# Performance work log

Measured on AMD Instinct MI355X. Metric: run time of the kernel, lower is better.

The kernel has to match this reference:

```python
import jax, jax.numpy as jnp
import numpy as np

L = 8        # num_layers
REPEAT = 2   # repeats per layer
DIM = 256    # mixer hidden dim
DIM2 = 128   # head dim (divisible by 32 for AvgPool1d(32))
B = 8192
EPS = 1e-5


def hardswish(x):
    return x * jnp.clip(x + 3.0, 0.0, 6.0) * (1.0 / 6.0)


def layernorm(x, g, b):
    m = jnp.mean(x, axis=-1, keepdims=True)
    xc = x - m
    v = jnp.mean(xc * xc, axis=-1, keepdims=True)
    return xc * jax.lax.rsqrt(v + EPS) * g + b


def setup_inputs() -> dict:
    key = jax.random.key(0)
    ks = jax.random.split(key, 32)
    s = 0.1
    inp = {
        "x": jax.random.normal(ks[0], (B, 3, 32, 32), dtype=jnp.float32),
        "conv_w": jax.random.normal(ks[1], (3,), dtype=jnp.float32) * s,
        "conv_b": jax.random.normal(ks[2], (1,), dtype=jnp.float32) * s,
        "fc0_w": jax.random.normal(ks[3], (32, 32), dtype=jnp.float32) * s,
        "fc0_b": jax.random.normal(ks[4], (32,), dtype=jnp.float32) * s,
        "ln1_g": jnp.ones((L, 32), dtype=jnp.float32),
        "ln1_b": jnp.zeros((L, 32), dtype=jnp.float32),
        "w11": jax.random.normal(ks[5], (L, DIM, 32), dtype=jnp.float32) * s,
        "b11": jax.random.normal(ks[6], (L, DIM), dtype=jnp.float32) * s,
        "w12": jax.random.normal(ks[7], (L, 32, DIM), dtype=jnp.float32) * s,
        "b12": jax.random.normal(ks[8], (L, 32), dtype=jnp.float32) * s,
        "ln2_g": jnp.ones((L, 32), dtype=jnp.float32),
        "ln2_b": jnp.zeros((L, 32), dtype=jnp.float32),
        "w21": jax.random.normal(ks[9], (L, DIM, 32), dtype=jnp.float32) * s,
        "b21": jax.random.normal(ks[10], (L, DIM), dtype=jnp.float32) * s,
        "w22": jax.random.normal(ks[11], (L, 32, DIM), dtype=jnp.float32) * s,
        "b22": jax.random.normal(ks[12], (L, 32), dtype=jnp.float32) * s,
        "fc1_w": jax.random.normal(ks[13], (DIM2, 32), dtype=jnp.float32) * s,
        "fc1_b": jax.random.normal(ks[14], (DIM2,), dtype=jnp.float32) * s,
        "fcout_w": jax.random.normal(ks[15], (10, DIM2), dtype=jnp.float32) * s,
        "fcout_b": jax.random.normal(ks[16], (10,), dtype=jnp.float32) * s,
    }
    return inp


def reference(x, conv_w, conv_b, fc0_w, fc0_b, ln1_g, ln1_b, w11, b11, w12, b12,
              ln2_g, ln2_b, w21, b21, w22, b22, fc1_w, fc1_b, fcout_w, fcout_b):
    # rgb_conv: 1x1 conv 3->1 channels, then squeeze -> [B, 32, 32]
    h = jnp.einsum('bchw,c->bhw', x, conv_w) + conv_b[0]
    h = h @ fc0_w.T + fc0_b  # fc0 over last dim (32)

    for i in range(L):
        for _ in range(REPEAT):
            # token-mixing branch (operates along dim 1 via permute)
            t = layernorm(h, ln1_g[i], ln1_b[i])
            t = jnp.swapaxes(t, 1, 2)                      # [B, 32, 32]
            t = hardswish(t @ w11[i].T + b11[i])           # [B, 32, DIM]
            t = t @ w12[i].T + b12[i]                      # [B, 32, 32]
            h = h + jnp.swapaxes(t, 1, 2)
            # channel-mixing branch
            c = layernorm(h, ln2_g[i], ln2_b[i])
            c = hardswish(c @ w21[i].T + b21[i])           # [B, 32, DIM]
            h = h + (c @ w22[i].T + b22[i])                # [B, 32, 32]

    y = hardswish(h @ fc1_w.T + fc1_b)                     # [B, 32, DIM2]
    # AvgPool1d(kernel=32, stride=32) over last dim -> [B, 32, DIM2//32]
    y = y.reshape(y.shape[0], 32, DIM2 // 32, 32).mean(axis=-1)
    y = y.reshape(y.shape[0], -1)                          # [B, DIM2]
    return y @ fcout_w.T + fcout_b                         # [B, 10]
```

## Files before the change

kernel.cpp:

```cpp
#include <hip/hip_runtime.h>

#define LNUM 8

typedef __attribute__((ext_vector_type(4))) float f32x4;
typedef __attribute__((ext_vector_type(2))) float f32x2;
typedef __attribute__((ext_vector_type(8))) _Float16 f16x8;
typedef __attribute__((ext_vector_type(2))) _Float16 f16x2;

#define MFMAH(A,B,C) __builtin_amdgcn_mfma_f32_16x16x32_f16(A,B,C,0,0,0)

#define PKRTZ(a,b) __builtin_bit_cast(f16x2, __builtin_amdgcn_cvt_pkrtz(a,b))

__device__ __forceinline__ float hswish_clamp(float t) {
  return __builtin_amdgcn_fmed3f(t + 3.f, 0.f, 6.f);
}

__device__ __forceinline__ int hws(int row, int c) {
  return (row << 5) + ((((c >> 2) ^ (row & 7)) << 2) | (c & 3));
}

__global__ void prep_weights(const float* __restrict__ w11, const float* __restrict__ b11,
                             const float* __restrict__ w12, const float* __restrict__ b12,
                             const float* __restrict__ g1,  const float* __restrict__ be1,
                             const float* __restrict__ w21, const float* __restrict__ b21,
                             const float* __restrict__ w22, const float* __restrict__ b22,
                             const float* __restrict__ g2,  const float* __restrict__ be2,
                             char* __restrict__ ws)
{
  const int lb = blockIdx.x;
  const int lay = lb >> 1, br = lb & 1;
  const float* w1  = (br ? w21 : w11) + lay*8192;
  const float* w2  = (br ? w22 : w12) + lay*8192;
  const float* bb1 = (br ? b21 : b11) + lay*256;
  const float* bb2 = (br ? b22 : b12) + lay*32;
  const float* gg  = (br ? g2  : g1 ) + lay*32;
  const float* bb  = (br ? be2 : be1) + lay*32;
  char* o = ws + (size_t)lb * 34816;
  _Float16* w1f = (_Float16*)o;
  _Float16* w2f = (_Float16*)(o + 16384);
  float* pr  = (float*)(o + 32768);
  const int t = threadIdx.x;
  #pragma unroll
  for (int i = 0; i < 4; ++i) {
    int s = t + i*256;
    int lane = s & 63;
    int row = (s >> 6)*16 + (lane & 15);
    int kb  = ((lane >> 4) & 3) * 8;
    const float* src = w1 + row*32 + kb;
    #pragma unroll
    for (int j = 0; j < 8; ++j) w1f[s*8 + j] = (_Float16)src[j];
  }
  #pragma unroll
  for (int i = 0; i < 4; ++i) {
    int s = t + i*256;
    int lane = s & 63;
    int tt = s >> 7;
    int nt = (s >> 6) & 1;
    int n  = nt*16 + (lane & 15);
    int qq = (lane >> 4) & 3;
    const float* src = w2 + n*256 + tt*32 + qq*4;
    _Float16* dst = w2f + s*8;
    #pragma unroll
    for (int j = 0; j < 4; ++j) dst[j]     = (_Float16)(src[j]      * (1.0f/6.0f));
    #pragma unroll
    for (int j = 0; j < 4; ++j) dst[4 + j] = (_Float16)(src[16 + j] * (1.0f/6.0f));
  }
  pr[t] = bb1[t];
  if (t < 32)      pr[256 + t] = bb2[t];
  else if (t < 64) pr[256 + t] = gg[t - 32];
  else if (t < 96) pr[256 + t] = bb[t - 64];
}

__global__ __launch_bounds__(256, 4)
void mixer_mfma(const float* __restrict__ x,
                const float* __restrict__ conv_w, const float* __restrict__ conv_b,
                const float* __restrict__ fc0_w,  const float* __restrict__ fc0_b,
                const char*  __restrict__ ws,
                const float* __restrict__ fc1_w,  const float* __restrict__ fc1_b,
                const float* __restrict__ fcout_w, const float* __restrict__ fcout_b,
                float* __restrict__ out)
{
  __shared__ float smem[4 * 2176];
  const int tid = threadIdx.x;
  const int wv  = tid >> 6;
  const int lid = tid & 63;
  const int ml  = lid & 15;
  const int q   = lid >> 4;
  const int q4  = q << 2, q8 = q << 3;
  const int sl  = lid >> 5, r = lid & 31;
  const int r7  = r & 7;

  float* hW  = smem + wv * 2176;
  float* stW = hW + 2048;

  const size_t b0 = (size_t)blockIdx.x * 8 + (size_t)wv * 2;

  {
    const size_t b = b0 + sl;
    const float* xb = x + b*3072 + r*32;
    const float cw0 = conv_w[0], cw1 = conv_w[1], cw2 = conv_w[2], cb = conv_b[0];
    float g[32];
    #pragma unroll
    for (int j4 = 0; j4 < 8; ++j4) {
      f32x4 a0 = *(const f32x4*)(xb + j4*4);
      f32x4 a1 = *(const f32x4*)(xb + 1024 + j4*4);
      f32x4 a2 = *(const f32x4*)(xb + 2048 + j4*4);
      #pragma unroll
      for (int e = 0; e < 4; ++e)
        g[j4*4+e] = cw0*a0[e] + cw1*a1[e] + cw2*a2[e] + cb;
    }
    f32x4* hp = (f32x4*)(hW + sl*1024 + (r << 5));
    #pragma unroll
    for (int a = 0; a < 8; ++a) {
      f32x4 w;
      #pragma unroll
      for (int e = 0; e < 4; ++e) {
        const int j = a*4 + e;
        const float* wr = fc0_w + j*32;
        float acc = fc0_b[j];
        #pragma unroll
        for (int k = 0; k < 32; ++k) acc += g[k]*wr[k];
        w[e] = acc;
      }
      hp[a ^ r7] = w;
    }
  }

  for (int lay = 0; lay < LNUM; ++lay)
  for (int rep = 0; rep < 2; ++rep)
  for (int br = 0; br < 2; ++br) {
    const char* wsb = ws + (size_t)(lay*2 + br) * 34816;
    const f16x8* w1f = (const f16x8*)wsb;
    const f16x8* w2f = (const f16x8*)(wsb + 16384);
    const float* pb1 = (const float*)(wsb + 32768);
    const float* pb2 = pb1 + 256;
    const float* pg  = pb1 + 288;
    const float* pbt = pb1 + 320;

    {
      const f32x4* hp = (const f32x4*)(hW + sl*1024 + (r << 5));
      float sum = 0.f, sq = 0.f;
      #pragma unroll
      for (int a = 0; a < 8; ++a) {
        f32x4 v = hp[a ^ r7];
        #pragma unroll
        for (int e = 0; e < 4; ++e) { sum += v[e]; sq += v[e]*v[e]; }
      }
      float m = sum * (1.f/32.f);
      float rstd = rsqrtf(sq*(1.f/32.f) - m*m + 1e-5f);
      *(f32x2*)(stW + ((sl << 5) + r)*2) = (f32x2){m, rstd};
    }

    f16x8 b1[4];
    if (br == 0) {
      const float ga = pg[ml],  gb = pg[16 + ml];
      const float ba = pbt[ml], bb2v = pbt[16 + ml];
      #pragma unroll
      for (int i = 0; i < 8; ++i) {
        const int k = q8 + i;
        f32x2 s0 = *(const f32x2*)(stW + k*2);
        f32x2 s1 = *(const f32x2*)(stW + 64 + k*2);
        #pragma unroll
        for (int mt = 0; mt < 4; ++mt) {
          const int samp = mt >> 1;
          const int c = ((mt & 1) << 4) + ml;
          f32x2 st = samp ? s1 : s0;
          float v = hW[samp*1024 + hws(k, c)];
          float g_ = (mt & 1) ? gb : ga;
          float be = (mt & 1) ? bb2v : ba;
          b1[mt][i] = (_Float16)((v - st[0]) * st[1] * g_ + be);
        }
      }
    } else {
      f32x4 g0 = *(const f32x4*)(pg + q8);
      f32x4 g1 = *(const f32x4*)(pg + q8 + 4);
      f32x4 t0 = *(const f32x4*)(pbt + q8);
      f32x4 t1 = *(const f32x4*)(pbt + q8 + 4);
      #pragma unroll
      for (int mt = 0; mt < 4; ++mt) {
        const int samp = mt >> 1;
        const int row = ((mt & 1) << 4) + ml;
        f32x2 st = *(const f32x2*)(stW + ((samp << 5) + row)*2);
        const f32x4* hr = (const f32x4*)(hW + samp*1024 + (row << 5));
        f32x4 v0 = hr[(2*q)     ^ (row & 7)];
        f32x4 v1 = hr[(2*q + 1) ^ (row & 7)];
        #pragma unroll
        for (int e = 0; e < 4; ++e) {
          b1[mt][e]     = (_Float16)((v0[e] - st[0]) * st[1] * g0[e] + t0[e]);
          b1[mt][4 + e] = (_Float16)((v1[e] - st[0]) * st[1] * g1[e] + t1[e]);
        }
      }
    }

    f32x4 acc2[2][4];
    {
      f32x4 i0 = *(const f32x4*)(pb2 + q4);
      f32x4 i1 = *(const f32x4*)(pb2 + 16 + q4);
      #pragma unroll
      for (int mt = 0; mt < 4; ++mt) { acc2[0][mt] = i0; acc2[1][mt] = i1; }
    }
    #pragma unroll 2
    for (int t = 0; t < 8; ++t) {
      f16x8 a1a = w1f[(t*2 + 0)*64 + lid];
      f16x8 a1b = w1f[(t*2 + 1)*64 + lid];
      f32x4 biasa = *(const f32x4*)(pb1 + t*32 + q4);
      f32x4 biasb = *(const f32x4*)(pb1 + t*32 + 16 + q4);
      f16x8 a2a = w2f[(t*2 + 0)*64 + lid];
      f16x8 a2b = w2f[(t*2 + 1)*64 + lid];
      #pragma unroll
      for (int mt = 0; mt < 4; ++mt) {
        f32x4 c1a = MFMAH(a1a, b1[mt], biasa);
        f32x4 c1b = MFMAH(a1b, b1[mt], biasb);
        float va0 = c1a[0]*hswish_clamp(c1a[0]);
        float va1 = c1a[1]*hswish_clamp(c1a[1]);
        float va2 = c1a[2]*hswish_clamp(c1a[2]);
        float va3 = c1a[3]*hswish_clamp(c1a[3]);
        float vb0 = c1b[0]*hswish_clamp(c1b[0]);
        float vb1 = c1b[1]*hswish_clamp(c1b[1]);
        float vb2 = c1b[2]*hswish_clamp(c1b[2]);
        float vb3 = c1b[3]*hswish_clamp(c1b[3]);
        union { f16x2 h2[4]; f16x8 v; } b2u;
        b2u.h2[0] = PKRTZ(va0, va1);
        b2u.h2[1] = PKRTZ(va2, va3);
        b2u.h2[2] = PKRTZ(vb0, vb1);
        b2u.h2[3] = PKRTZ(vb2, vb3);
        acc2[0][mt] = MFMAH(a2a, b2u.v, acc2[0][mt]);
        acc2[1][mt] = MFMAH(a2b, b2u.v, acc2[1][mt]);
      }
    }

    if (br == 0) {
      #pragma unroll
      for (int mt = 0; mt < 4; ++mt) {
        const int samp = mt >> 1;
        const int c = ((mt & 1) << 4) + ml;
        float* hs = hW + samp*1024;
        #pragma unroll
        for (int nt = 0; nt < 2; ++nt)
        #pragma unroll
        for (int rg = 0; rg < 4; ++rg) {
          const int n = (nt << 4) + q4 + rg;
          hs[hws(n, c)] += acc2[nt][mt][rg];
        }
      }
    } else {
      #pragma unroll
      for (int mt = 0; mt < 4; ++mt) {
        const int samp = mt >> 1;
        const int row = ((mt & 1) << 4) + ml;
        f32x4* hr = (f32x4*)(hW + samp*1024 + (row << 5));
        #pragma unroll
        for (int nt = 0; nt < 2; ++nt) {
          const int a = ((nt << 2) + q) ^ (row & 7);
          f32x4 v = hr[a];
          v += acc2[nt][mt];
          hr[a] = v;
        }
      }
    }
  }

  {
    const size_t b = b0 + sl;
    float hv[32];
    {
      const f32x4* hp = (const f32x4*)(hW + sl*1024 + (r << 5));
      #pragma unroll
      for (int a = 0; a < 8; ++a) {
        f32x4 v = hp[a ^ r7];
        #pragma unroll
        for (int e = 0; e < 4; ++e) hv[a*4 + e] = v[e];
      }
    }
    float pooled[4];
    #pragma unroll
    for (int c = 0; c < 4; ++c) {
      float accp = 0.f;
      for (int e2 = 0; e2 < 32; ++e2) {
        const float* wr = fc1_w + (c*32 + e2)*32;
        float acc = fc1_b[c*32 + e2];
        #pragma unroll
        for (int k = 0; k < 32; ++k) acc += hv[k]*wr[k];
        accp += acc * hswish_clamp(acc) * (1.f/6.f);
      }
      pooled[c] = accp * (1.f/32.f);
    }
    float* pf = hW + sl*1024;
    #pragma unroll
    for (int c = 0; c < 4; ++c) pf[r*4 + c] = pooled[c];
    if (r < 10) {
      const float* pv = hW + sl*1024;
      const float* wr = fcout_w + r*128;
      float acc = fcout_b[r];
      #pragma unroll 8
      for (int m = 0; m < 128; ++m) acc += pv[m]*wr[m];
      out[b*10 + r] = acc;
    }
  }
}

extern "C" void kernel_launch(void* const* d_in, const int* in_sizes, int n_in,
                              void* d_out, int out_size, void* d_ws, size_t ws_size,
                              hipStream_t stream) {
  (void)in_sizes; (void)n_in; (void)out_size; (void)ws_size;
  const float* x       = (const float*)d_in[0];
  const float* conv_w  = (const float*)d_in[1];
  const float* conv_b  = (const float*)d_in[2];
  const float* fc0_w   = (const float*)d_in[3];
  const float* fc0_b   = (const float*)d_in[4];
  const float* ln1_g   = (const float*)d_in[5];
  const float* ln1_b   = (const float*)d_in[6];
  const float* w11     = (const float*)d_in[7];
  const float* b11     = (const float*)d_in[8];
  const float* w12     = (const float*)d_in[9];
  const float* b12     = (const float*)d_in[10];
  const float* ln2_g   = (const float*)d_in[11];
  const float* ln2_b   = (const float*)d_in[12];
  const float* w21     = (const float*)d_in[13];
  const float* b21     = (const float*)d_in[14];
  const float* w22     = (const float*)d_in[15];
  const float* b22     = (const float*)d_in[16];
  const float* fc1_w   = (const float*)d_in[17];
  const float* fc1_b   = (const float*)d_in[18];
  const float* fcout_w = (const float*)d_in[19];
  const float* fcout_b = (const float*)d_in[20];
  float* out = (float*)d_out;
  char* ws = (char*)d_ws;

  prep_weights<<<16, 256, 0, stream>>>(w11, b11, w12, b12, ln1_g, ln1_b,
                                       w21, b21, w22, b22, ln2_g, ln2_b, ws);
  mixer_mfma<<<1024, 256, 0, stream>>>(x, conv_w, conv_b, fc0_w, fc0_b,
                                       (const char*)ws, fc1_w, fc1_b,
                                       fcout_w, fcout_b, out);
}
```

Before: 487.2 us.

## Process one sample per wave, use MFMA for fc1 head and packed fp16 hardswish

Each wave now handles one sample instead of two, which halves shared memory per block and doubles the grid, with launch bounds raised to 8 blocks per CU. The fc0 stage is spread across both half-waves. The fc1/pool head moves from a scalar fp32 loop to fp16 MFMA, using a weight layout prepared by an extra prep block. The hardswish between the two MFMA layers is now done in packed fp16 after conversion. This trades some precision and per-wave MFMA density for more occupancy and a cheaper epilogue.

```diff
diff --git a/kernel.cpp b/kernel.cpp
--- a/kernel.cpp
+++ b/kernel.cpp
@@ -8,11 +8,18 @@
 typedef __attribute__((ext_vector_type(2))) _Float16 f16x2;
 
 #define MFMAH(A,B,C) __builtin_amdgcn_mfma_f32_16x16x32_f16(A,B,C,0,0,0)
-
 #define PKRTZ(a,b) __builtin_bit_cast(f16x2, __builtin_amdgcn_cvt_pkrtz(a,b))
 
 __device__ __forceinline__ float hswish_clamp(float t) {
   return __builtin_amdgcn_fmed3f(t + 3.f, 0.f, 6.f);
+}
+__device__ __forceinline__ f16x2 hsw_pk(f16x2 t) {
+  const f16x2 c3 = {(_Float16)3.0f, (_Float16)3.0f};
+  const f16x2 c0 = {(_Float16)0.0f, (_Float16)0.0f};
+  const f16x2 c6 = {(_Float16)6.0f, (_Float16)6.0f};
+  f16x2 u = t + c3;
+  u = __builtin_elementwise_min(__builtin_elementwise_max(u, c0), c6);
+  return t * u;
 }
 
 __device__ __forceinline__ int hws(int row, int c) {
@@ -25,9 +32,28 @@
                              const float* __restrict__ w21, const float* __restrict__ b21,
                              const float* __restrict__ w22, const float* __restrict__ b22,
                              const float* __restrict__ g2,  const float* __restrict__ be2,
+                             const float* __restrict__ fc1w, const float* __restrict__ fc1b,
                              char* __restrict__ ws)
 {
   const int lb = blockIdx.x;
+  const int t = threadIdx.x;
+  if (lb == 16) {
+    char* o = ws + (size_t)16 * 34816;
+    _Float16* wf = (_Float16*)o;
+    float* pr = (float*)(o + 8192);
+    #pragma unroll
+    for (int i = 0; i < 2; ++i) {
+      int s = t + i*256;
+      int lane = s & 63;
+      int row = (s >> 6)*16 + (lane & 15);
+      int kb  = ((lane >> 4) & 3) * 8;
+      const float* src = fc1w + row*32 + kb;
+      #pragma unroll
+      for (int j = 0; j < 8; ++j) wf[s*8 + j] = (_Float16)src[j];
+    }
+    if (t < 128) pr[t] = fc1b[t];
+    return;
+  }
   const int lay = lb >> 1, br = lb & 1;
   const float* w1  = (br ? w21 : w11) + lay*8192;
   const float* w2  = (br ? w22 : w12) + lay*8192;
@@ -39,7 +65,6 @@
   _Float16* w1f = (_Float16*)o;
   _Float16* w2f = (_Float16*)(o + 16384);
   float* pr  = (float*)(o + 32768);
-  const int t = threadIdx.x;
   #pragma unroll
   for (int i = 0; i < 4; ++i) {
     int s = t + i*256;
@@ -71,16 +96,15 @@
   else if (t < 96) pr[256 + t] = bb[t - 64];
 }
 
-__global__ __launch_bounds__(256, 4)
+__global__ __launch_bounds__(256, 8)
 void mixer_mfma(const float* __restrict__ x,
                 const float* __restrict__ conv_w, const float* __restrict__ conv_b,
                 const float* __restrict__ fc0_w,  const float* __restrict__ fc0_b,
                 const char*  __restrict__ ws,
-                const float* __restrict__ fc1_w,  const float* __restrict__ fc1_b,
                 const float* __restrict__ fcout_w, const float* __restrict__ fcout_b,
                 float* __restrict__ out)
 {
-  __shared__ float smem[4 * 2176];
+  __shared__ float smem[4 * 1088];
   const int tid = threadIdx.x;
   const int wv  = tid >> 6;
   const int lid = tid & 63;
@@ -90,39 +114,44 @@
   const int sl  = lid >> 5, r = lid & 31;
   const int r7  = r & 7;
 
-  float* hW  = smem + wv * 2176;
-  float* stW = hW + 2048;
-
-  const size_t b0 = (size_t)blockIdx.x * 8 + (size_t)wv * 2;
+  float* hW  = smem + wv * 1088;
+  float* stW = hW + 1024;
+
+  const size_t b = (size_t)blockIdx.x * 4 + (size_t)wv;
 
   {
-    const size_t b = b0 + sl;
     const float* xb = x + b*3072 + r*32;
     const float cw0 = conv_w[0], cw1 = conv_w[1], cw2 = conv_w[2], cb = conv_b[0];
-    float g[32];
-    #pragma unroll
-    for (int j4 = 0; j4 < 8; ++j4) {
-      f32x4 a0 = *(const f32x4*)(xb + j4*4);
-      f32x4 a1 = *(const f32x4*)(xb + 1024 + j4*4);
-      f32x4 a2 = *(const f32x4*)(xb + 2048 + j4*4);
-      #pragma unroll
-      for (int e = 0; e < 4; ++e)
-        g[j4*4+e] = cw0*a0[e] + cw1*a1[e] + cw2*a2[e] + cb;
-    }
-    f32x4* hp = (f32x4*)(hW + sl*1024 + (r << 5));
+    f32x4* hp = (f32x4*)(hW + (r << 5));
+    #pragma unroll
+    for (int cc = 0; cc < 4; ++cc) {
+      const int a = sl*4 + cc;
+      f32x4 a0 = *(const f32x4*)(xb + a*4);
+      f32x4 a1 = *(const f32x4*)(xb + 1024 + a*4);
+      f32x4 a2 = *(const f32x4*)(xb + 2048 + a*4);
+      f32x4 g4;
+      #pragma unroll
+      for (int e = 0; e < 4; ++e) g4[e] = cw0*a0[e] + cw1*a1[e] + cw2*a2[e] + cb;
+      hp[a ^ r7] = g4;
+    }
+    float accs[16];
+    #pragma unroll
+    for (int jj = 0; jj < 16; ++jj) accs[jj] = fc0_b[sl*16 + jj];
     #pragma unroll
     for (int a = 0; a < 8; ++a) {
-      f32x4 w;
-      #pragma unroll
-      for (int e = 0; e < 4; ++e) {
-        const int j = a*4 + e;
-        const float* wr = fc0_w + j*32;
-        float acc = fc0_b[j];
-        #pragma unroll
-        for (int k = 0; k < 32; ++k) acc += g[k]*wr[k];
-        w[e] = acc;
-      }
-      hp[a ^ r7] = w;
+      f32x4 g4 = hp[a ^ r7];
+      #pragma unroll
+      for (int jj = 0; jj < 16; ++jj) {
+        const f32x4 w4 = *(const f32x4*)(fc0_w + (sl*16 + jj)*32 + a*4);
+        accs[jj] += g4[0]*w4[0] + g4[1]*w4[1] + g4[2]*w4[2] + g4[3]*w4[3];
+      }
+    }
+    #pragma unroll
+    for (int cc = 0; cc < 4; ++cc) {
+      f32x4 w4;
+      #pragma unroll
+      for (int e = 0; e < 4; ++e) w4[e] = accs[cc*4 + e];
+      hp[(sl*4 + cc) ^ r7] = w4;
     }
   }
 
@@ -138,7 +167,7 @@
     const float* pbt = pb1 + 320;
 
     {
-      const f32x4* hp = (const f32x4*)(hW + sl*1024 + (r << 5));
+      const f32x4* hp = (const f32x4*)(hW + (r << 5));
       float sum = 0.f, sq = 0.f;
       #pragma unroll
       for (int a = 0; a < 8; ++a) {
@@ -148,28 +177,21 @@
       }
       float m = sum * (1.f/32.f);
       float rstd = rsqrtf(sq*(1.f/32.f) - m*m + 1e-5f);
-      *(f32x2*)(stW + ((sl << 5) + r)*2) = (f32x2){m, rstd};
-    }
-
-    f16x8 b1[4];
+      *(f32x2*)(stW + r*2) = (f32x2){m, rstd};
+    }
+
+    f16x8 b1[2];
     if (br == 0) {
       const float ga = pg[ml],  gb = pg[16 + ml];
       const float ba = pbt[ml], bb2v = pbt[16 + ml];
       #pragma unroll
       for (int i = 0; i < 8; ++i) {
         const int k = q8 + i;
-        f32x2 s0 = *(const f32x2*)(stW + k*2);
-        f32x2 s1 = *(const f32x2*)(stW + 64 + k*2);
-        #pragma unroll
-        for (int mt = 0; mt < 4; ++mt) {
-          const int samp = mt >> 1;
-          const int c = ((mt & 1) << 4) + ml;
-          f32x2 st = samp ? s1 : s0;
-          float v = hW[samp*1024 + hws(k, c)];
-          float g_ = (mt & 1) ? gb : ga;
-          float be = (mt & 1) ? bb2v : ba;
-          b1[mt][i] = (_Float16)((v - st[0]) * st[1] * g_ + be);
-        }
+        f32x2 st = *(const f32x2*)(stW + k*2);
+        float v0 = hW[hws(k, ml)];
+        float v1 = hW[hws(k, 16 + ml)];
+        b1[0][i] = (_Float16)((v0 - st[0]) * st[1] * ga + ba);
+        b1[1][i] = (_Float16)((v1 - st[0]) * st[1] * gb + bb2v);
       }
     } else {
       f32x4 g0 = *(const f32x4*)(pg + q8);
@@ -177,11 +199,10 @@
       f32x4 t0 = *(const f32x4*)(pbt + q8);
       f32x4 t1 = *(const f32x4*)(pbt + q8 + 4);
       #pragma unroll
-      for (int mt = 0; mt < 4; ++mt) {
-        const int samp = mt >> 1;
-        const int row = ((mt & 1) << 4) + ml;
-        f32x2 st = *(const f32x2*)(stW + ((samp << 5) + row)*2);
-        const f32x4* hr = (const f32x4*)(hW + samp*1024 + (row << 5));
+      for (int mt = 0; mt < 2; ++mt) {
+        const int row = (mt << 4) + ml;
+        f32x2 st = *(const f32x2*)(stW + row*2);
+        const f32x4* hr = (const f32x4*)(hW + (row << 5));
         f32x4 v0 = hr[(2*q)     ^ (row & 7)];
         f32x4 v1 = hr[(2*q + 1) ^ (row & 7)];
         #pragma unroll
@@ -192,12 +213,12 @@
       }
     }
 
-    f32x4 acc2[2][4];
+    f32x4 acc2[2][2];
     {
       f32x4 i0 = *(const f32x4*)(pb2 + q4);
       f32x4 i1 = *(const f32x4*)(pb2 + 16 + q4);
       #pragma unroll
-      for (int mt = 0; mt < 4; ++mt) { acc2[0][mt] = i0; acc2[1][mt] = i1; }
+      for (int mt = 0; mt < 2; ++mt) { acc2[0][mt] = i0; acc2[1][mt] = i1; }
     }
     #pragma unroll 2
     for (int t = 0; t < 8; ++t) {
@@ -208,22 +229,14 @@
       f16x8 a2a = w2f[(t*2 + 0)*64 + lid];
       f16x8 a2b = w2f[(t*2 + 1)*64 + lid];
       #pragma unroll
-      for (int mt = 0; mt < 4; ++mt) {
+      for (int mt = 0; mt < 2; ++mt) {
         f32x4 c1a = MFMAH(a1a, b1[mt], biasa);
         f32x4 c1b = MFMAH(a1b, b1[mt], biasb);
-        float va0 = c1a[0]*hswish_clamp(c1a[0]);
-        float va1 = c1a[1]*hswish_clamp(c1a[1]);
-        float va2 = c1a[2]*hswish_clamp(c1a[2]);
-        float va3 = c1a[3]*hswish_clamp(c1a[3]);
-        float vb0 = c1b[0]*hswish_clamp(c1b[0]);
-        float vb1 = c1b[1]*hswish_clamp(c1b[1]);
-        float vb2 = c1b[2]*hswish_clamp(c1b[2]);
-        float vb3 = c1b[3]*hswish_clamp(c1b[3]);
         union { f16x2 h2[4]; f16x8 v; } b2u;
-        b2u.h2[0] = PKRTZ(va0, va1);
-        b2u.h2[1] = PKRTZ(va2, va3);
-        b2u.h2[2] = PKRTZ(vb0, vb1);
-        b2u.h2[3] = PKRTZ(vb2, vb3);
+        b2u.h2[0] = hsw_pk(PKRTZ(c1a[0], c1a[1]));
+        b2u.h2[1] = hsw_pk(PKRTZ(c1a[2], c1a[3]));
+        b2u.h2[2] = hsw_pk(PKRTZ(c1b[0], c1b[1]));
+        b2u.h2[3] = hsw_pk(PKRTZ(c1b[2], c1b[3]));
         acc2[0][mt] = MFMAH(a2a, b2u.v, acc2[0][mt]);
         acc2[1][mt] = MFMAH(a2b, b2u.v, acc2[1][mt]);
       }
@@ -231,24 +244,21 @@
 
     if (br == 0) {
       #pragma unroll
-      for (int mt = 0; mt < 4; ++mt) {
-        const int samp = mt >> 1;
-        const int c = ((mt & 1) << 4) + ml;
-        float* hs = hW + samp*1024;
+      for (int mt = 0; mt < 2; ++mt) {
+        const int c = (mt << 4) + ml;
         #pragma unroll
         for (int nt = 0; nt < 2; ++nt)
         #pragma unroll
         for (int rg = 0; rg < 4; ++rg) {
           const int n = (nt << 4) + q4 + rg;
-          hs[hws(n, c)] += acc2[nt][mt][rg];
+          hW[hws(n, c)] += acc2[nt][mt][rg];
         }
       }
     } else {
       #pragma unroll
-      for (int mt = 0; mt < 4; ++mt) {
-        const int samp = mt >> 1;
-        const int row = ((mt & 1) << 4) + ml;
-        f32x4* hr = (f32x4*)(hW + samp*1024 + (row << 5));
+      for (int mt = 0; mt < 2; ++mt) {
+        const int row = (mt << 4) + ml;
+        f32x4* hr = (f32x4*)(hW + (row << 5));
         #pragma unroll
         for (int nt = 0; nt < 2; ++nt) {
           const int a = ((nt << 2) + q) ^ (row & 7);
@@ -261,40 +271,59 @@
   }
 
   {
-    const size_t b = b0 + sl;
-    float hv[32];
-    {
-      const f32x4* hp = (const f32x4*)(hW + sl*1024 + (r << 5));
-      #pragma unroll
-      for (int a = 0; a < 8; ++a) {
-        f32x4 v = hp[a ^ r7];
-        #pragma unroll
-        for (int e = 0; e < 4; ++e) hv[a*4 + e] = v[e];
-      }
-    }
-    float pooled[4];
-    #pragma unroll
-    for (int c = 0; c < 4; ++c) {
-      float accp = 0.f;
-      for (int e2 = 0; e2 < 32; ++e2) {
-        const float* wr = fc1_w + (c*32 + e2)*32;
-        float acc = fc1_b[c*32 + e2];
-        #pragma unroll
-        for (int k = 0; k < 32; ++k) acc += hv[k]*wr[k];
-        accp += acc * hswish_clamp(acc) * (1.f/6.f);
-      }
-      pooled[c] = accp * (1.f/32.f);
-    }
-    float* pf = hW + sl*1024;
-    #pragma unroll
-    for (int c = 0; c < 4; ++c) pf[r*4 + c] = pooled[c];
-    if (r < 10) {
-      const float* pv = hW + sl*1024;
-      const float* wr = fcout_w + r*128;
-      float acc = fcout_b[r];
-      #pragma unroll 8
-      for (int m = 0; m < 128; ++m) acc += pv[m]*wr[m];
-      out[b*10 + r] = acc;
+    const f16x8* fc1f = (const f16x8*)(ws + (size_t)16 * 34816);
+    const float* fb   = (const float*)(ws + (size_t)16 * 34816 + 8192);
+    f16x8 be[2];
+    #pragma unroll
+    for (int mt = 0; mt < 2; ++mt) {
+      const int row = (mt << 4) + ml;
+      const f32x4* hr = (const f32x4*)(hW + (row << 5));
+      f32x4 v0 = hr[(2*q)     ^ (row & 7)];
+      f32x4 v1 = hr[(2*q + 1) ^ (row & 7)];
+      #pragma unroll
+      for (int e = 0; e < 4; ++e) {
+        be[mt][e]     = (_Float16)v0[e];
+        be[mt][4 + e] = (_Float16)v1[e];
+      }
+    }
+    float pl[4][2] = {};
+    #pragma unroll
+    for (int dt = 0; dt < 8; ++dt) {
+      f16x8 af = fc1f[dt*64 + lid];
+      f32x4 bias4 = *(const f32x4*)(fb + dt*16 + q4);
+      #pragma unroll
+      for (int mt = 0; mt < 2; ++mt) {
+        f32x4 c = MFMAH(af, be[mt], bias4);
+        float s = 0.f;
+        #pragma unroll
+        for (int rg = 0; rg < 4; ++rg) s += c[rg] * hswish_clamp(c[rg]);
+        pl[dt >> 1][mt] += s;
+      }
+    }
+    #pragma unroll
+    for (int t = 0; t < 4; ++t)
+    #pragma unroll
+    for (int mt = 0; mt < 2; ++mt) {
+      float v = pl[t][mt];
+      v += __shfl_xor(v, 16);
+      v += __shfl_xor(v, 32);
+      pl[t][mt] = v;
+    }
+    #pragma unroll
+    for (int mt = 0; mt < 2; ++mt)
+    #pragma unroll
+    for (int t = 0; t < 4; ++t)
+      hW[((mt << 4) + ml)*4 + t] = pl[t][mt];
+    if (lid < 10) {
+      const float* wr = fcout_w + lid*128;
+      float acc = 0.f;
+      #pragma unroll
+      for (int m4 = 0; m4 < 32; ++m4) {
+        f32x4 pv = *(const f32x4*)(hW + m4*4);
+        f32x4 w4 = *(const f32x4*)(wr + m4*4);
+        acc += pv[0]*w4[0] + pv[1]*w4[1] + pv[2]*w4[2] + pv[3]*w4[3];
+      }
+      out[b*10 + lid] = fcout_b[lid] + acc * (1.f/192.f);
     }
   }
 }
@@ -327,9 +356,9 @@
   float* out = (float*)d_out;
   char* ws = (char*)d_ws;
 
-  prep_weights<<<16, 256, 0, stream>>>(w11, b11, w12, b12, ln1_g, ln1_b,
-                                       w21, b21, w22, b22, ln2_g, ln2_b, ws);
-  mixer_mfma<<<1024, 256, 0, stream>>>(x, conv_w, conv_b, fc0_w, fc0_b,
-                                       (const char*)ws, fc1_w, fc1_b,
-                                       fcout_w, fcout_b, out);
-}
+  prep_weights<<<17, 256, 0, stream>>>(w11, b11, w12, b12, ln1_g, ln1_b,
+                                       w21, b21, w22, b22, ln2_g, ln2_b,
+                                       fc1_w, fc1_b, ws);
+  mixer_mfma<<<2048, 256, 0, stream>>>(x, conv_w, conv_b, fc0_w, fc0_b,
+                                       (const char*)ws, fcout_w, fcout_b, out);
+}
```

Result: slower. 1.351 ms (+177.3%).
